# Kernel tuning notes

Measured on AMD Instinct MI355X. Metric: run time of the kernel, lower is better.

Reference implementation:

```python
import jax, jax.numpy as jnp
import numpy as np

NUM_HEADS = 12

def setup_inputs() -> dict:
    key = jax.random.key(0)
    ks = jax.random.split(key, 11)
    H = 768
    N, B = 512, 16
    s = 0.02
    return {
        "x": jax.random.normal(ks[0], (N, B, H), dtype=jnp.float32),
        "attention_bias": jax.random.normal(ks[1], (B, NUM_HEADS, N, N), dtype=jnp.float32),
        "key_padding_mask": jnp.zeros((B, N), dtype=bool),
        "Wq": jax.random.normal(ks[2], (H, H), dtype=jnp.float32) * s,
        "bq": jax.random.normal(ks[3], (H,), dtype=jnp.float32) * s,
        "Wk": jax.random.normal(ks[4], (H, H), dtype=jnp.float32) * s,
        "bk": jax.random.normal(ks[5], (H,), dtype=jnp.float32) * s,
        "Wv": jax.random.normal(ks[6], (H, H), dtype=jnp.float32) * s,
        "bv": jax.random.normal(ks[7], (H,), dtype=jnp.float32) * s,
        "Wo": jax.random.normal(ks[8], (H, H), dtype=jnp.float32) * s,
        "bo": jax.random.normal(ks[9], (H,), dtype=jnp.float32) * s,
    }

def reference(x, attention_bias, key_padding_mask, Wq, bq, Wk, bk, Wv, bv, Wo, bo):
    N, B, H = x.shape
    nh = NUM_HEADS
    hd = H // nh
    scaling = hd ** -0.5
    # projections (nodes-first layout), then -> (B, nh, N, hd)
    def split_heads(t):
        return t.reshape(N, B, nh, hd).transpose(1, 2, 0, 3)
    q = split_heads(x @ Wq + bq)
    k = split_heads(x @ Wk + bk)
    v = split_heads(x @ Wv + bv)
    scores = jnp.einsum('bhnd,bhmd->bhnm', q, k) * scaling + attention_bias
    scores = jnp.where(key_padding_mask[:, None, None, :], -jnp.inf, scores)
    attn = jax.nn.softmax(scores, axis=-1)  # dropout_rate=0.0 -> identity
    out = jnp.einsum('bhnm,bhmd->bhnd', attn, v)
    out = out.transpose(2, 0, 1, 3).reshape(N, B, H)
    return out @ Wo + bo
```

## Files before the change

### kernel.cpp

```cpp
#include <hip/hip_runtime.h>
#include <stdint.h>

typedef __attribute__((ext_vector_type(8))) short bf16x8;
typedef __attribute__((ext_vector_type(4))) float f32x4;

#define GLB(p) ((__attribute__((address_space(1))) void*)(p))
#define LDSP(p) ((__attribute__((address_space(3))) void*)(p))

__device__ __forceinline__ unsigned short f2bf(float f) {
  union { float f; unsigned u; } v; v.f = f;
  unsigned r = v.u + 0x7fffu + ((v.u >> 16) & 1u);
  return (unsigned short)(r >> 16);
}

__global__ __launch_bounds__(256) void k_convert_x(const float* __restrict__ x,
                                                   unsigned short* __restrict__ X) {
  int i = blockIdx.x * 256 + threadIdx.x;
  float4 v = ((const float4*)x)[i];
  ushort4 o;
  o.x = f2bf(v.x); o.y = f2bf(v.y); o.z = f2bf(v.z); o.w = f2bf(v.w);
  ((ushort4*)X)[i] = o;
}

__global__ __launch_bounds__(256) void k_transpose_w(const float* __restrict__ src,
                                                     unsigned short* __restrict__ dst) {
  __shared__ float t[32][33];
  int tx = threadIdx.x & 31, ty = threadIdx.x >> 5;
  int c0 = blockIdx.x * 32, r0 = blockIdx.y * 32;
  #pragma unroll
  for (int i = 0; i < 4; ++i)
    t[ty + i * 8][tx] = src[(size_t)(r0 + ty + i * 8) * 768 + c0 + tx];
  __syncthreads();
  #pragma unroll
  for (int i = 0; i < 4; ++i)
    dst[(size_t)(c0 + ty + i * 8) * 768 + r0 + tx] = f2bf(t[tx][ty + i * 8]);
}

__global__ __launch_bounds__(256) void k_transpose_v(const unsigned short* __restrict__ V,
                                                     unsigned short* __restrict__ VT) {
  __shared__ unsigned short t[32][33];
  int tx = threadIdx.x & 31, ty = threadIdx.x >> 5;
  int c0 = blockIdx.x * 32;
  int r0 = blockIdx.y * 32;
  int bh = blockIdx.z;
  const unsigned short* src = V + (size_t)bh * 512 * 64;
  unsigned short* dst = VT + (size_t)bh * 64 * 512;
  #pragma unroll
  for (int i = 0; i < 4; ++i)
    t[ty + i * 8][tx] = src[(r0 + ty + i * 8) * 64 + c0 + tx];
  __syncthreads();
  #pragma unroll
  for (int i = 0; i < 4; ++i)
    dst[(c0 + ty + i * 8) * 512 + r0 + tx] = t[tx][ty + i * 8];
}

template <int EPI>
__global__ __launch_bounds__(256) void k_gemm(
    const unsigned short* __restrict__ A, const unsigned short* __restrict__ Bt,
    const float* __restrict__ b0, const float* __restrict__ b1, const float* __restrict__ b2,
    unsigned short* __restrict__ Qo, unsigned short* __restrict__ Ko,
    unsigned short* __restrict__ Vo, float* __restrict__ Co) {
  __shared__ unsigned short sA[128 * 32];
  __shared__ unsigned short sB[128 * 32];
  const int tid = threadIdx.x, lane = tid & 63, wid = tid >> 6;
  const int wr = wid >> 1, wc = wid & 1;
  const int m0 = blockIdx.y * 128, n0 = blockIdx.x * 128;
  const int lrow = lane >> 2, lkoff = (lane & 3) * 8;
  const int fr = lane & 15, fg = lane >> 4;
  f32x4 acc[4][4] = {};

  for (int k0 = 0; k0 < 768; k0 += 32) {
    #pragma unroll
    for (int it = 0; it < 2; ++it) {
      int rb = it * 64 + wid * 16;
      __builtin_amdgcn_global_load_lds(GLB(A + (size_t)(m0 + rb + lrow) * 768 + k0 + lkoff),
                                       LDSP(sA + rb * 32), 16, 0, 0);
      __builtin_amdgcn_global_load_lds(GLB(Bt + (size_t)(n0 + rb + lrow) * 768 + k0 + lkoff),
                                       LDSP(sB + rb * 32), 16, 0, 0);
    }
    __syncthreads();
    bf16x8 af[4], bw[4];
    #pragma unroll
    for (int f = 0; f < 4; ++f) {
      af[f] = *(const bf16x8*)&sA[(wr * 64 + f * 16 + fr) * 32 + fg * 8];
      bw[f] = *(const bf16x8*)&sB[(wc * 64 + f * 16 + fr) * 32 + fg * 8];
    }
    #pragma unroll
    for (int i = 0; i < 4; ++i)
      #pragma unroll
      for (int j = 0; j < 4; ++j)
        acc[i][j] = __builtin_amdgcn_mfma_f32_16x16x32_bf16(af[i], bw[j], acc[i][j], 0, 0, 0);
    __syncthreads();
  }

  if (EPI == 0) {
    #pragma unroll
    for (int fm = 0; fm < 4; ++fm) {
      int row0 = m0 + wr * 64 + fm * 16;
      int nseq = row0 >> 4;
      #pragma unroll
      for (int fn = 0; fn < 4; ++fn) {
        int col = n0 + wc * 64 + fn * 16 + fr;
        int sel = (col >= 1536) ? 2 : (col >= 768) ? 1 : 0;
        int jj = col - sel * 768;
        int h = jj >> 6, d = jj & 63;
        const float* bp = (sel == 0) ? b0 : (sel == 1) ? b1 : b2;
        float bias = bp[jj];
        unsigned short* dst = (sel == 0) ? Qo : (sel == 1) ? Ko : Vo;
        #pragma unroll
        for (int r = 0; r < 4; ++r) {
          int bb = fg * 4 + r;
          dst[(((size_t)bb * 12 + h) * 512 + nseq) * 64 + d] = f2bf(acc[fm][fn][r] + bias);
        }
      }
    }
  } else {
    #pragma unroll
    for (int fm = 0; fm < 4; ++fm) {
      int row0 = m0 + wr * 64 + fm * 16;
      #pragma unroll
      for (int fn = 0; fn < 4; ++fn) {
        int col = n0 + wc * 64 + fn * 16 + fr;
        float bias = b0[col];
        #pragma unroll
        for (int r = 0; r < 4; ++r)
          Co[(size_t)(row0 + fg * 4 + r) * 768 + col] = acc[fm][fn][r] + bias;
      }
    }
  }
}

__global__ __launch_bounds__(256) void k_attn(
    const unsigned short* __restrict__ Q, const unsigned short* __restrict__ K,
    const unsigned short* __restrict__ VT, const float* __restrict__ bias,
    const unsigned char* __restrict__ mask, unsigned short* __restrict__ O) {
  __shared__ unsigned short P[4][16 * 512];
  const int tid = threadIdx.x, lane = tid & 63, wid = tid >> 6;
  const int bh = blockIdx.x >> 3, qt = blockIdx.x & 7;
  const int b = bh / 12, h = bh - b * 12;
  const int q0 = qt * 64 + wid * 16;
  const int fr = lane & 15, fg = lane >> 4;
  const unsigned short* Qb = Q + (size_t)bh * 512 * 64;
  const unsigned short* Kb = K + (size_t)bh * 512 * 64;
  const unsigned short* Vb = VT + (size_t)bh * 64 * 512;
  const float* Bb = bias + ((size_t)bh * 512 + q0) * 512;
  const unsigned char* mb = mask + b * 512;

  bf16x8 aq0 = *(const bf16x8*)&Qb[(q0 + fr) * 64 + fg * 8];
  bf16x8 aq1 = *(const bf16x8*)&Qb[(q0 + fr) * 64 + fg * 8 + 32];

  float s[32][4];
  #pragma unroll
  for (int t = 0; t < 32; ++t) {
    bf16x8 kb0 = *(const bf16x8*)&Kb[(t * 16 + fr) * 64 + fg * 8];
    bf16x8 kb1 = *(const bf16x8*)&Kb[(t * 16 + fr) * 64 + fg * 8 + 32];
    f32x4 a = {};
    a = __builtin_amdgcn_mfma_f32_16x16x32_bf16(aq0, kb0, a, 0, 0, 0);
    a = __builtin_amdgcn_mfma_f32_16x16x32_bf16(aq1, kb1, a, 0, 0, 0);
    int col = t * 16 + fr;
    float madd = mb[col] ? -1e30f : 0.0f;
    #pragma unroll
    for (int r = 0; r < 4; ++r)
      s[t][r] = a[r] * 0.125f + Bb[(fg * 4 + r) * 512 + col] + madd;
  }

  unsigned short* Pw = &P[wid][0];
  #pragma unroll
  for (int r = 0; r < 4; ++r) {
    float m = s[0][r];
    #pragma unroll
    for (int t = 1; t < 32; ++t) m = fmaxf(m, s[t][r]);
    #pragma unroll
    for (int o = 1; o < 16; o <<= 1) m = fmaxf(m, __shfl_xor(m, o, 16));
    float l = 0.0f;
    #pragma unroll
    for (int t = 0; t < 32; ++t) { float p = __expf(s[t][r] - m); s[t][r] = p; l += p; }
    #pragma unroll
    for (int o = 1; o < 16; o <<= 1) l += __shfl_xor(l, o, 16);
    float inv = 1.0f / l;
    int row = fg * 4 + r, swz = (row & 7) << 4;
    #pragma unroll
    for (int t = 0; t < 32; ++t) {
      int cb = (t * 16 + fr) * 2;
      *(unsigned short*)((char*)Pw + row * 1024 + (cb ^ swz)) = f2bf(s[t][r] * inv);
    }
  }
  __syncthreads();

  f32x4 o4[4] = {};
  {
    int row = fr, swz = (row & 7) << 4;
    #pragma unroll
    for (int kt = 0; kt < 16; ++kt) {
      bf16x8 pa = *(const bf16x8*)((char*)Pw + row * 1024 + ((fg * 16 + kt * 64) ^ swz));
      #pragma unroll
      for (int dt = 0; dt < 4; ++dt) {
        bf16x8 vb = *(const bf16x8*)&Vb[(size_t)(dt * 16 + fr) * 512 + kt * 32 + fg * 8];
        o4[dt] = __builtin_amdgcn_mfma_f32_16x16x32_bf16(pa, vb, o4[dt], 0, 0, 0);
      }
    }
  }
  #pragma unroll
  for (int dt = 0; dt < 4; ++dt)
    #pragma unroll
    for (int r = 0; r < 4; ++r)
      O[(size_t)((q0 + fg * 4 + r) * 16 + b) * 768 + h * 64 + dt * 16 + fr] = f2bf(o4[dt][r]);
}

extern "C" void kernel_launch(void* const* d_in, const int* in_sizes, int n_in,
                              void* d_out, int out_size, void* d_ws, size_t ws_size,
                              hipStream_t stream) {
  const float* x = (const float*)d_in[0];
  const float* ab = (const float*)d_in[1];
  const unsigned char* mask = (const unsigned char*)d_in[2];
  const float* Wq = (const float*)d_in[3];
  const float* bq = (const float*)d_in[4];
  const float* Wk = (const float*)d_in[5];
  const float* bk = (const float*)d_in[6];
  const float* Wv = (const float*)d_in[7];
  const float* bv = (const float*)d_in[8];
  const float* Wo = (const float*)d_in[9];
  const float* bo = (const float*)d_in[10];
  float* out = (float*)d_out;

  char* w = (char*)d_ws;
  unsigned short* X   = (unsigned short*)(w);
  unsigned short* WTq = (unsigned short*)(w + 12582912);
  unsigned short* WoT = (unsigned short*)(w + 16121856);
  unsigned short* Qb  = (unsigned short*)(w + 17301504);
  unsigned short* Kb  = (unsigned short*)(w + 29884416);
  unsigned short* Vn  = (unsigned short*)(w + 42467328);
  unsigned short* VT  = (unsigned short*)(w + 55050240);
  unsigned short* O   = X;

  k_convert_x<<<6144, 256, 0, stream>>>(x, X);
  dim3 tg(24, 24);
  k_transpose_w<<<tg, 256, 0, stream>>>(Wq, WTq);
  k_transpose_w<<<tg, 256, 0, stream>>>(Wk, WTq + 768 * 768);
  k_transpose_w<<<tg, 256, 0, stream>>>(Wv, WTq + 2 * 768 * 768);
  k_transpose_w<<<tg, 256, 0, stream>>>(Wo, WoT);
  k_gemm<0><<<dim3(18, 64), 256, 0, stream>>>(X, WTq, bq, bk, bv, Qb, Kb, Vn, nullptr);
  k_transpose_v<<<dim3(2, 16, 192), 256, 0, stream>>>(Vn, VT);
  k_attn<<<1536, 256, 0, stream>>>(Qb, Kb, VT, ab, mask, O);
  k_gemm<1><<<dim3(6, 64), 256, 0, stream>>>(O, WoT, bo, nullptr, nullptr, nullptr, nullptr, nullptr, out);
}
```

Before: 458.3 us.

## Restructure attention into chunked online softmax with transposed score MFMA

The attention kernel now processes keys in four chunks of 128 with an online (running max/sum) softmax instead of holding all 512 scores per row in registers. The score MFMA operands are swapped so each lane holds contiguous key columns, which allows vectorized float4 nontemporal bias loads that are prefetched one chunk ahead. The P tile in LDS shrinks to a small double buffer per wave, and normalization is deferred to the final output. The output-projection stores become nontemporal. This cuts register and LDS pressure and overlaps the bias stream with compute, at the cost of extra rescaling and shuffle work per chunk.

Result: slower. 477.4 us (+4.2%).

```diff
diff --git a/kernel.cpp b/kernel.cpp
--- a/kernel.cpp
+++ b/kernel.cpp
@@ -2,6 +2,7 @@
 #include <stdint.h>
 
 typedef __attribute__((ext_vector_type(8))) short bf16x8;
+typedef __attribute__((ext_vector_type(4))) short bf16x4;
 typedef __attribute__((ext_vector_type(4))) float f32x4;
 
 #define GLB(p) ((__attribute__((address_space(1))) void*)(p))
@@ -124,7 +125,8 @@
         float bias = b0[col];
         #pragma unroll
         for (int r = 0; r < 4; ++r)
-          Co[(size_t)(row0 + fg * 4 + r) * 768 + col] = acc[fm][fn][r] + bias;
+          __builtin_nontemporal_store(acc[fm][fn][r] + bias,
+                                      &Co[(size_t)(row0 + fg * 4 + r) * 768 + col]);
       }
     }
   }
@@ -134,7 +136,7 @@
     const unsigned short* __restrict__ Q, const unsigned short* __restrict__ K,
     const unsigned short* __restrict__ VT, const float* __restrict__ bias,
     const unsigned char* __restrict__ mask, unsigned short* __restrict__ O) {
-  __shared__ unsigned short P[4][16 * 512];
+  __shared__ unsigned short P[4][2][512];
   const int tid = threadIdx.x, lane = tid & 63, wid = tid >> 6;
   const int bh = blockIdx.x >> 3, qt = blockIdx.x & 7;
   const int b = bh / 12, h = bh - b * 12;
@@ -143,68 +145,102 @@
   const unsigned short* Qb = Q + (size_t)bh * 512 * 64;
   const unsigned short* Kb = K + (size_t)bh * 512 * 64;
   const unsigned short* Vb = VT + (size_t)bh * 64 * 512;
-  const float* Bb = bias + ((size_t)bh * 512 + q0) * 512;
+  const float* biasRow = bias + ((size_t)bh * 512 + q0 + fr) * 512 + fg * 4;
   const unsigned char* mb = mask + b * 512;
 
   bf16x8 aq0 = *(const bf16x8*)&Qb[(q0 + fr) * 64 + fg * 8];
   bf16x8 aq1 = *(const bf16x8*)&Qb[(q0 + fr) * 64 + fg * 8 + 32];
 
-  float s[32][4];
-  #pragma unroll
-  for (int t = 0; t < 32; ++t) {
-    bf16x8 kb0 = *(const bf16x8*)&Kb[(t * 16 + fr) * 64 + fg * 8];
-    bf16x8 kb1 = *(const bf16x8*)&Kb[(t * 16 + fr) * 64 + fg * 8 + 32];
-    f32x4 a = {};
-    a = __builtin_amdgcn_mfma_f32_16x16x32_bf16(aq0, kb0, a, 0, 0, 0);
-    a = __builtin_amdgcn_mfma_f32_16x16x32_bf16(aq1, kb1, a, 0, 0, 0);
-    int col = t * 16 + fr;
-    float madd = mb[col] ? -1e30f : 0.0f;
-    #pragma unroll
-    for (int r = 0; r < 4; ++r)
-      s[t][r] = a[r] * 0.125f + Bb[(fg * 4 + r) * 512 + col] + madd;
-  }
-
-  unsigned short* Pw = &P[wid][0];
+  float m_run = -1e30f, l_run = 0.0f;
+  f32x4 o4[4] = {};
+  const int swz = (fr & 7) << 3;
+
+  f32x4 bv[8];
+  #pragma unroll
+  for (int t = 0; t < 8; ++t)
+    bv[t] = __builtin_nontemporal_load((const f32x4*)(biasRow + t * 16));
+
+  #pragma unroll 1
+  for (int c = 0; c < 4; ++c) {
+    float s[8][4];
+    #pragma unroll
+    for (int t = 0; t < 8; ++t) {
+      int kr = (c * 8 + t) * 16 + fr;
+      bf16x8 kb0 = *(const bf16x8*)&Kb[kr * 64 + fg * 8];
+      bf16x8 kb1 = *(const bf16x8*)&Kb[kr * 64 + fg * 8 + 32];
+      f32x4 a = {};
+      a = __builtin_amdgcn_mfma_f32_16x16x32_bf16(kb0, aq0, a, 0, 0, 0);
+      a = __builtin_amdgcn_mfma_f32_16x16x32_bf16(kb1, aq1, a, 0, 0, 0);
+      uchar4 mk = *(const uchar4*)&mb[(c * 8 + t) * 16 + fg * 4];
+      s[t][0] = a[0] * 0.125f + bv[t][0] + (mk.x ? -1e30f : 0.0f);
+      s[t][1] = a[1] * 0.125f + bv[t][1] + (mk.y ? -1e30f : 0.0f);
+      s[t][2] = a[2] * 0.125f + bv[t][2] + (mk.z ? -1e30f : 0.0f);
+      s[t][3] = a[3] * 0.125f + bv[t][3] + (mk.w ? -1e30f : 0.0f);
+    }
+    if (c < 3) {
+      #pragma unroll
+      for (int t = 0; t < 8; ++t)
+        bv[t] = __builtin_nontemporal_load((const f32x4*)(biasRow + (c + 1) * 128 + t * 16));
+    }
+    float cm = s[0][0];
+    #pragma unroll
+    for (int t = 0; t < 8; ++t)
+      #pragma unroll
+      for (int r = 0; r < 4; ++r) cm = fmaxf(cm, s[t][r]);
+    cm = fmaxf(cm, __shfl_xor(cm, 16));
+    cm = fmaxf(cm, __shfl_xor(cm, 32));
+    float mnew = fmaxf(m_run, cm);
+    float fac = __expf(m_run - mnew);
+    float csum = 0.0f;
+    #pragma unroll
+    for (int t = 0; t < 8; ++t)
+      #pragma unroll
+      for (int r = 0; r < 4; ++r) {
+        float p = __expf(s[t][r] - mnew);
+        s[t][r] = p; csum += p;
+      }
+    csum += __shfl_xor(csum, 16);
+    csum += __shfl_xor(csum, 32);
+    l_run = l_run * fac + csum;
+    m_run = mnew;
+    #pragma unroll
+    for (int r = 0; r < 4; ++r) {
+      float f = __shfl(fac, fg * 4 + r);
+      #pragma unroll
+      for (int dt = 0; dt < 4; ++dt) o4[dt][r] *= f;
+    }
+    #pragma unroll
+    for (int ks = 0; ks < 4; ++ks) {
+      unsigned short* Pw = &P[wid][ks & 1][0];
+      #pragma unroll
+      for (int tp = 0; tp < 2; ++tp) {
+        int tl = ks * 2 + tp;
+        ushort4 pk4;
+        pk4.x = f2bf(s[tl][0]); pk4.y = f2bf(s[tl][1]);
+        pk4.z = f2bf(s[tl][2]); pk4.w = f2bf(s[tl][3]);
+        *(ushort4*)((char*)Pw + ((fr * 64 + tp * 32 + fg * 8) ^ swz)) = pk4;
+      }
+      bf16x4 plo = *(const bf16x4*)((char*)Pw + ((fr * 64 + fg * 16) ^ swz));
+      bf16x4 phi = *(const bf16x4*)((char*)Pw + ((fr * 64 + fg * 16 + 8) ^ swz));
+      bf16x8 pa = __builtin_shufflevector(plo, phi, 0, 1, 2, 3, 4, 5, 6, 7);
+      int kglob = c * 128 + ks * 32;
+      #pragma unroll
+      for (int dt = 0; dt < 4; ++dt) {
+        bf16x8 vb = *(const bf16x8*)&Vb[(size_t)(dt * 16 + fr) * 512 + kglob + fg * 8];
+        o4[dt] = __builtin_amdgcn_mfma_f32_16x16x32_bf16(pa, vb, o4[dt], 0, 0, 0);
+      }
+    }
+  }
+
+  float inv = 1.0f / l_run;
   #pragma unroll
   for (int r = 0; r < 4; ++r) {
-    float m = s[0][r];
-    #pragma unroll
-    for (int t = 1; t < 32; ++t) m = fmaxf(m, s[t][r]);
-    #pragma unroll
-    for (int o = 1; o < 16; o <<= 1) m = fmaxf(m, __shfl_xor(m, o, 16));
-    float l = 0.0f;
-    #pragma unroll
-    for (int t = 0; t < 32; ++t) { float p = __expf(s[t][r] - m); s[t][r] = p; l += p; }
-    #pragma unroll
-    for (int o = 1; o < 16; o <<= 1) l += __shfl_xor(l, o, 16);
-    float inv = 1.0f / l;
-    int row = fg * 4 + r, swz = (row & 7) << 4;
-    #pragma unroll
-    for (int t = 0; t < 32; ++t) {
-      int cb = (t * 16 + fr) * 2;
-      *(unsigned short*)((char*)Pw + row * 1024 + (cb ^ swz)) = f2bf(s[t][r] * inv);
-    }
-  }
-  __syncthreads();
-
-  f32x4 o4[4] = {};
-  {
-    int row = fr, swz = (row & 7) << 4;
-    #pragma unroll
-    for (int kt = 0; kt < 16; ++kt) {
-      bf16x8 pa = *(const bf16x8*)((char*)Pw + row * 1024 + ((fg * 16 + kt * 64) ^ swz));
-      #pragma unroll
-      for (int dt = 0; dt < 4; ++dt) {
-        bf16x8 vb = *(const bf16x8*)&Vb[(size_t)(dt * 16 + fr) * 512 + kt * 32 + fg * 8];
-        o4[dt] = __builtin_amdgcn_mfma_f32_16x16x32_bf16(pa, vb, o4[dt], 0, 0, 0);
-      }
-    }
-  }
-  #pragma unroll
-  for (int dt = 0; dt < 4; ++dt)
-    #pragma unroll
-    for (int r = 0; r < 4; ++r)
-      O[(size_t)((q0 + fg * 4 + r) * 16 + b) * 768 + h * 64 + dt * 16 + fr] = f2bf(o4[dt][r]);
+    float iv = __shfl(inv, fg * 4 + r);
+    #pragma unroll
+    for (int dt = 0; dt < 4; ++dt)
+      O[(size_t)((q0 + fg * 4 + r) * 16 + b) * 768 + h * 64 + dt * 16 + fr] =
+          f2bf(o4[dt][r] * iv);
+  }
 }
 
 extern "C" void kernel_launch(void* const* d_in, const int* in_sizes, int n_in,
```
